# Performance work log

Measured on AMD Instinct MI355X. Metric: run time of the kernel, lower is better.

Reference implementation:

```python
import jax, jax.numpy as jnp
jax.config.update("jax_enable_x64", True)
import numpy as np

BATCH, N = 8192, 4096
EPS = 1e-6
NR_ITERS = 5  # Newton-Raphson iterations in the gate circuit


def setup_inputs() -> dict:
    key = jax.random.key(0)
    x = jax.random.normal(key, (BATCH, N), dtype=jnp.float32)
    return {"x": x}


def reference(x):
    # Faithful numeric emulation of the bit-pulse FP64 gate circuit.
    # The original encodes each scalar as 32 bit-pulses, widens to FP64,
    # and runs the exact arithmetic below on FP64 values, then narrows
    # back to FP32. We operate on the decoded floats directly.
    x64 = x.astype(jnp.float64)                      # FP32ToFP64Converter
    mean = jnp.mean(x64, axis=-1, keepdims=True)     # sum via FP64 adders / N
    c = x64 - mean                                   # x + (-mean) via sign NOT + adder
    var = jnp.mean(c * c, axis=-1, keepdims=True)    # FP64 squares, summed, / N
    vpe = var + EPS
    # rsqrt via Newton-Raphson, seeded with y0 = 1/(var+eps) (FP64 divider)
    y = 1.0 / vpe
    for _ in range(NR_ITERS):
        y = 0.5 * y * (3.0 - vpe * (y * y))
    out = c * y                                      # normalize
    return out.astype(jnp.float32)                   # FP64ToFP32Converter
```

## Files before the change

### kernel.cpp

```cpp
#include <hip/hip_runtime.h>


#define LN_BATCH 8192
#define LN_N     4096
#define LN_WPB   4
#define LN_THREADS (LN_WPB * 64)
#define LN_F4PT  16
#define LN_EPS   1e-6

typedef float vfloat4 __attribute__((ext_vector_type(4)));

__device__ __forceinline__ double wave_allreduce_add(double s) {
#pragma unroll
    for (int off = 1; off < 64; off <<= 1)
        s += __shfl_xor(s, off, 64);
    return s;
}

__global__ __launch_bounds__(LN_THREADS)
void spike_layernorm_kernel(const float* __restrict__ x, float* __restrict__ out) {
    const int wave = threadIdx.x >> 6;
    const int lane = threadIdx.x & 63;
    const int row  = blockIdx.x * LN_WPB + wave;

    const vfloat4* __restrict__ xr =
        reinterpret_cast<const vfloat4*>(x + (size_t)row * LN_N);
    vfloat4* __restrict__ orow =
        reinterpret_cast<vfloat4*>(out + (size_t)row * LN_N);

    vfloat4 v[LN_F4PT];
#pragma unroll
    for (int i = 0; i < LN_F4PT; ++i)
        v[i] = __builtin_nontemporal_load(&xr[lane + i * 64]);

    double s0 = 0.0, s1 = 0.0, s2 = 0.0, s3 = 0.0;
#pragma unroll
    for (int i = 0; i < LN_F4PT; i += 4) {
        s0 += (double)v[i + 0].x + (double)v[i + 0].y + (double)v[i + 0].z + (double)v[i + 0].w;
        s1 += (double)v[i + 1].x + (double)v[i + 1].y + (double)v[i + 1].z + (double)v[i + 1].w;
        s2 += (double)v[i + 2].x + (double)v[i + 2].y + (double)v[i + 2].z + (double)v[i + 2].w;
        s3 += (double)v[i + 3].x + (double)v[i + 3].y + (double)v[i + 3].z + (double)v[i + 3].w;
    }
    const double mean = wave_allreduce_add((s0 + s1) + (s2 + s3)) * (1.0 / LN_N);

    double q0 = 0.0, q1 = 0.0, q2 = 0.0, q3 = 0.0;
#pragma unroll
    for (int i = 0; i < LN_F4PT; i += 4) {
        double d;
        d = (double)v[i + 0].x - mean; q0 += d * d;
        d = (double)v[i + 0].y - mean; q0 += d * d;
        d = (double)v[i + 0].z - mean; q0 += d * d;
        d = (double)v[i + 0].w - mean; q0 += d * d;
        d = (double)v[i + 1].x - mean; q1 += d * d;
        d = (double)v[i + 1].y - mean; q1 += d * d;
        d = (double)v[i + 1].z - mean; q1 += d * d;
        d = (double)v[i + 1].w - mean; q1 += d * d;
        d = (double)v[i + 2].x - mean; q2 += d * d;
        d = (double)v[i + 2].y - mean; q2 += d * d;
        d = (double)v[i + 2].z - mean; q2 += d * d;
        d = (double)v[i + 2].w - mean; q2 += d * d;
        d = (double)v[i + 3].x - mean; q3 += d * d;
        d = (double)v[i + 3].y - mean; q3 += d * d;
        d = (double)v[i + 3].z - mean; q3 += d * d;
        d = (double)v[i + 3].w - mean; q3 += d * d;
    }
    const double var = wave_allreduce_add((q0 + q1) + (q2 + q3)) * (1.0 / LN_N);

    const double vpe = var + LN_EPS;
    double y = 1.0 / vpe;
#pragma unroll
    for (int it = 0; it < 5; ++it)
        y = 0.5 * y * (3.0 - vpe * (y * y));

#pragma unroll
    for (int i = 0; i < LN_F4PT; ++i) {
        vfloat4 o;
        o.x = (float)(((double)v[i].x - mean) * y);
        o.y = (float)(((double)v[i].y - mean) * y);
        o.z = (float)(((double)v[i].z - mean) * y);
        o.w = (float)(((double)v[i].w - mean) * y);
        __builtin_nontemporal_store(o, &orow[lane + i * 64]);
    }
}

extern "C" void kernel_launch(void* const* d_in, const int* in_sizes, int n_in,
                              void* d_out, int out_size, void* d_ws, size_t ws_size,
                              hipStream_t stream) {
    const float* x = (const float*)d_in[0];
    float* out = (float*)d_out;
    spike_layernorm_kernel<<<LN_BATCH / LN_WPB, LN_THREADS, 0, stream>>>(x, out);
}
```

Baseline: 220.7 us.

## Compute mean and variance in one pass and reload row for normalize

Replaces the two-pass mean and centered-variance computation with a single pass that accumulates sum and sum of squares in FP64, then derives the variance as E[x^2]-mean^2. The two wave reductions are merged into one shuffle loop. The row is no longer held in 64 registers; it is read once for the statistics and read again with nontemporal loads for normalization. This lowers register pressure and removes a dependent pass, at the cost of a second global read of each row (likely served from cache) and a numerically different variance formula.

```diff
diff --git a/kernel.cpp b/kernel.cpp
--- a/kernel.cpp
+++ b/kernel.cpp
@@ -10,13 +10,6 @@
 
 typedef float vfloat4 __attribute__((ext_vector_type(4)));
 
-__device__ __forceinline__ double wave_allreduce_add(double s) {
-#pragma unroll
-    for (int off = 1; off < 64; off <<= 1)
-        s += __shfl_xor(s, off, 64);
-    return s;
-}
-
 __global__ __launch_bounds__(LN_THREADS)
 void spike_layernorm_kernel(const float* __restrict__ x, float* __restrict__ out) {
     const int wave = threadIdx.x >> 6;
@@ -28,45 +21,44 @@
     vfloat4* __restrict__ orow =
         reinterpret_cast<vfloat4*>(out + (size_t)row * LN_N);
 
-    vfloat4 v[LN_F4PT];
-#pragma unroll
-    for (int i = 0; i < LN_F4PT; ++i)
-        v[i] = __builtin_nontemporal_load(&xr[lane + i * 64]);
-
     double s0 = 0.0, s1 = 0.0, s2 = 0.0, s3 = 0.0;
-#pragma unroll
-    for (int i = 0; i < LN_F4PT; i += 4) {
-        s0 += (double)v[i + 0].x + (double)v[i + 0].y + (double)v[i + 0].z + (double)v[i + 0].w;
-        s1 += (double)v[i + 1].x + (double)v[i + 1].y + (double)v[i + 1].z + (double)v[i + 1].w;
-        s2 += (double)v[i + 2].x + (double)v[i + 2].y + (double)v[i + 2].z + (double)v[i + 2].w;
-        s3 += (double)v[i + 3].x + (double)v[i + 3].y + (double)v[i + 3].z + (double)v[i + 3].w;
-    }
-    const double mean = wave_allreduce_add((s0 + s1) + (s2 + s3)) * (1.0 / LN_N);
-
     double q0 = 0.0, q1 = 0.0, q2 = 0.0, q3 = 0.0;
 #pragma unroll
     for (int i = 0; i < LN_F4PT; i += 4) {
-        double d;
-        d = (double)v[i + 0].x - mean; q0 += d * d;
-        d = (double)v[i + 0].y - mean; q0 += d * d;
-        d = (double)v[i + 0].z - mean; q0 += d * d;
-        d = (double)v[i + 0].w - mean; q0 += d * d;
-        d = (double)v[i + 1].x - mean; q1 += d * d;
-        d = (double)v[i + 1].y - mean; q1 += d * d;
-        d = (double)v[i + 1].z - mean; q1 += d * d;
-        d = (double)v[i + 1].w - mean; q1 += d * d;
-        d = (double)v[i + 2].x - mean; q2 += d * d;
-        d = (double)v[i + 2].y - mean; q2 += d * d;
-        d = (double)v[i + 2].z - mean; q2 += d * d;
-        d = (double)v[i + 2].w - mean; q2 += d * d;
-        d = (double)v[i + 3].x - mean; q3 += d * d;
-        d = (double)v[i + 3].y - mean; q3 += d * d;
-        d = (double)v[i + 3].z - mean; q3 += d * d;
-        d = (double)v[i + 3].w - mean; q3 += d * d;
+        vfloat4 a = xr[lane + (i + 0) * 64];
+        vfloat4 b = xr[lane + (i + 1) * 64];
+        vfloat4 c = xr[lane + (i + 2) * 64];
+        vfloat4 d = xr[lane + (i + 3) * 64];
+        double t;
+        t = (double)a.x; s0 += t; q0 = fma(t, t, q0);
+        t = (double)a.y; s0 += t; q0 = fma(t, t, q0);
+        t = (double)a.z; s0 += t; q0 = fma(t, t, q0);
+        t = (double)a.w; s0 += t; q0 = fma(t, t, q0);
+        t = (double)b.x; s1 += t; q1 = fma(t, t, q1);
+        t = (double)b.y; s1 += t; q1 = fma(t, t, q1);
+        t = (double)b.z; s1 += t; q1 = fma(t, t, q1);
+        t = (double)b.w; s1 += t; q1 = fma(t, t, q1);
+        t = (double)c.x; s2 += t; q2 = fma(t, t, q2);
+        t = (double)c.y; s2 += t; q2 = fma(t, t, q2);
+        t = (double)c.z; s2 += t; q2 = fma(t, t, q2);
+        t = (double)c.w; s2 += t; q2 = fma(t, t, q2);
+        t = (double)d.x; s3 += t; q3 = fma(t, t, q3);
+        t = (double)d.y; s3 += t; q3 = fma(t, t, q3);
+        t = (double)d.z; s3 += t; q3 = fma(t, t, q3);
+        t = (double)d.w; s3 += t; q3 = fma(t, t, q3);
     }
-    const double var = wave_allreduce_add((q0 + q1) + (q2 + q3)) * (1.0 / LN_N);
+    double s = (s0 + s1) + (s2 + s3);
+    double q = (q0 + q1) + (q2 + q3);
 
-    const double vpe = var + LN_EPS;
+#pragma unroll
+    for (int off = 1; off < 64; off <<= 1) {
+        s += __shfl_xor(s, off, 64);
+        q += __shfl_xor(q, off, 64);
+    }
+
+    const double mean = s * (1.0 / LN_N);
+    const double var  = fma(-mean, mean, q * (1.0 / LN_N));
+    const double vpe  = var + LN_EPS;
     double y = 1.0 / vpe;
 #pragma unroll
     for (int it = 0; it < 5; ++it)
@@ -74,11 +66,12 @@
 
 #pragma unroll
     for (int i = 0; i < LN_F4PT; ++i) {
+        vfloat4 a = __builtin_nontemporal_load(&xr[lane + i * 64]);
         vfloat4 o;
-        o.x = (float)(((double)v[i].x - mean) * y);
-        o.y = (float)(((double)v[i].y - mean) * y);
-        o.z = (float)(((double)v[i].z - mean) * y);
-        o.w = (float)(((double)v[i].w - mean) * y);
+        o.x = (float)(((double)a.x - mean) * y);
+        o.y = (float)(((double)a.y - mean) * y);
+        o.z = (float)(((double)a.z - mean) * y);
+        o.w = (float)(((double)a.w - mean) * y);
         __builtin_nontemporal_store(o, &orow[lane + i * 64]);
     }
 }
```

Measured after the change: 232.7 us. +5.5%, slower.
